# Optimization experiments

Measured on AMD Instinct MI355X. Metric: run time of the kernel, lower is better.

## Reference

```python
import jax, jax.numpy as jnp
import numpy as np
from jax import lax

G = 8        # group_num
BS = 32      # blocksize
SC = 13      # sample_channel = round(32*32*0.1/8)


def conv2d(x, w, b=None, stride=1, pad=0):
    y = lax.conv_general_dilated(x, w, (stride, stride), [(pad, pad), (pad, pad)],
                                 dimension_numbers=("NCHW", "OIHW", "NCHW"))
    if b is not None:
        y = y + b[None, :, None, None]
    return y


def prelu(x, a):
    return jnp.where(x >= 0, x, a * x)


def depth_to_space(x, bs):
    # matches Reshape_Concat_Adap: channel index = c_out*bs*bs + i*bs + j
    b, c, h, w = x.shape
    co = c // (bs * bs)
    x = x.reshape(b, co, bs, bs, h, w)
    x = x.transpose(0, 1, 4, 2, 5, 3)  # b, co, h, bs, w, bs
    return x.reshape(b, co, h * bs, w * bs)


def setup_inputs() -> dict:
    key = jax.random.key(0)
    ks = jax.random.split(key, 16)
    s = 0.05
    inp = {
        "x": jax.random.normal(ks[0], (8, 1, 256, 256), jnp.float32),
        "sample_w": jax.random.normal(ks[1], (G, SC, 1, BS, BS), jnp.float32) * 0.02,
        "up_w": jax.random.normal(ks[2], (G, BS * BS, SC, 1, 1), jnp.float32) * s,
        "up_b": jnp.zeros((G, BS * BS), jnp.float32),
        "conv1_w": jax.random.normal(ks[3], (G, 64, 1, 3, 3), jnp.float32) * s,
        "conv1_b": jnp.zeros((G, 64), jnp.float32),
        "conv1_a": jnp.full((G,), 0.25, jnp.float32),
        "fus_w": jax.random.normal(ks[4], (G - 1, 64, 128, 3, 3), jnp.float32) * s,
        "fus_b": jnp.zeros((G - 1, 64), jnp.float32),
        "fus_a": jnp.full((G - 1,), 0.25, jnp.float32),
        "t2_w": jax.random.normal(ks[5], (G, 64, 64, 3, 3), jnp.float32) * s,
        "t2_b": jnp.zeros((G, 64), jnp.float32),
        "t2_a": jnp.full((G,), 0.25, jnp.float32),
        "t3_w": jax.random.normal(ks[6], (G, 64, 64, 3, 3), jnp.float32) * s,
        "t3_b": jnp.zeros((G, 64), jnp.float32),
        "t3_a": jnp.full((G,), 0.25, jnp.float32),
        "t4_w": jax.random.normal(ks[7], (G, 64, 64, 3, 3), jnp.float32) * s,
        "t4_b": jnp.zeros((G, 64), jnp.float32),
        "t4_a": jnp.full((G,), 0.25, jnp.float32),
        "t5_w": jax.random.normal(ks[8], (G, 1, 64, 3, 3), jnp.float32) * s,
        "t5_b": jnp.zeros((G, 1), jnp.float32),
    }
    return inp


def reference(x, sample_w, up_w, up_b, conv1_w, conv1_b, conv1_a,
              fus_w, fus_b, fus_a, t2_w, t2_b, t2_a, t3_w, t3_b, t3_a,
              t4_w, t4_b, t4_a, t5_w, t5_b):
    def head(g):
        y = conv2d(x, sample_w[g], stride=BS)              # [B,SC,H/32,W/32]
        y = conv2d(y, up_w[g], up_b[g])                    # [B,1024,H/32,W/32]
        y = depth_to_space(y, BS)                          # [B,1,H,W]
        return prelu(conv2d(y, conv1_w[g], conv1_b[g], pad=1), conv1_a[g])

    def tail(h, g):
        h = prelu(conv2d(h, t2_w[g], t2_b[g], pad=1), t2_a[g])
        h = prelu(conv2d(h, t3_w[g], t3_b[g], pad=1), t3_a[g])
        h = prelu(conv2d(h, t4_w[g], t4_b[g], pad=1), t4_a[g])
        return conv2d(h, t5_w[g], t5_b[g], pad=1)          # [B,1,H,W]

    heads = [head(g) for g in range(G)]
    cur = heads[0]
    outs = [tail(cur, 0)]
    for m in range(G - 1):
        cat = jnp.concatenate([cur, heads[m + 1]], axis=1)  # [B,128,H,W]
        cur = prelu(conv2d(cat, fus_w[m], fus_b[m], pad=1), fus_a[m])
        outs.append(tail(cur, m + 1))
    return jnp.stack(outs, axis=0)  # [G,B,1,H,W]
```

## Files before the change

kernel.cpp:

```cpp
#include <hip/hip_runtime.h>
#include <stdint.h>

typedef __attribute__((ext_vector_type(8))) short short8;
typedef __attribute__((ext_vector_type(16))) float floatx16;

#define PLANE 16777216

__device__ __forceinline__ float b2f(short s) {
  union { uint32_t u; float f; } v; v.u = ((uint32_t)(uint16_t)s) << 16; return v.f;
}
__device__ __forceinline__ short f2b(float f) {
  union { float f; uint32_t u; } v; v.f = f;
  uint32_t r = (v.u + 0x7FFFu + ((v.u >> 16) & 1u)) >> 16;
  return (short)r;
}

__device__ __forceinline__ uint32_t ldsAddr(int r, int xp, int c) {
  uint32_t byte = ((uint32_t)(r * 258 + xp) << 6) + ((uint32_t)c << 1);
  byte ^= ((uint32_t)(xp & 7)) << 4;
  return byte;
}

template<int NCHUNK>
__global__ __launch_bounds__(512, 2)
void k_conv(const short* __restrict__ in1, const short* __restrict__ in2,
            const short* __restrict__ wp, const float* __restrict__ bias,
            const float* __restrict__ alpha, short* __restrict__ out)
{
  __shared__ __align__(16) uint8_t smem[4 * 258 * 64];
  const int wg = blockIdx.x;
  const int b = wg & 7;
  const int y0 = (wg >> 3) * 2;
  const int tid = threadIdx.x;
  const int l = tid & 63;
  const int w = tid >> 6;
  const int yrow = w & 1;
  const int pxq = w >> 1;
  const int lm = l & 31;
  const int lh = l >> 5;

  floatx16 acc[4];
  #pragma unroll
  for (int mf = 0; mf < 4; ++mf)
    #pragma unroll
    for (int r = 0; r < 16; ++r) acc[mf][r] = 0.f;

  const int xbase = pxq * 64 + lm;

  short8 stg[8];

  auto issue = [&](int q) {
    const short* __restrict__ src = ((q < 2) ? in1 : in2) + (size_t)(q & 1) * PLANE;
    #pragma unroll
    for (int i = 0; i < 8; ++i) {
      int widx = tid + i * 512;
      int r = widx >> 10;
      int xp = ((widx >> 2) & 255) + 1;
      int co = (widx & 3) << 3;
      int yy = y0 + r - 1;
      short8 v = {0, 0, 0, 0, 0, 0, 0, 0};
      if ((unsigned)yy < 256u)
        v = *(const short8*)(src + ((b * 256 + yy) * 256 + (xp - 1)) * 32 + co);
      stg[i] = v;
    }
  };
  auto commit = [&]() {
    #pragma unroll
    for (int i = 0; i < 8; ++i) {
      int widx = tid + i * 512;
      int r = widx >> 10;
      int xp = ((widx >> 2) & 255) + 1;
      int co = (widx & 3) << 3;
      *(short8*)(smem + ldsAddr(r, xp, co)) = stg[i];
    }
  };

  if (tid < 32) {
    short8 z = {0, 0, 0, 0, 0, 0, 0, 0};
    int r = tid >> 3;
    int xp = (tid & 4) ? 257 : 0;
    int co = (tid & 3) << 3;
    *(short8*)(smem + ldsAddr(r, xp, co)) = z;
  }

  issue(0);
  commit();
  __syncthreads();

  #pragma unroll
  for (int q = 0; q < NCHUNK; ++q) {
    if (q + 1 < NCHUNK) issue(q + 1);

    __builtin_amdgcn_s_setprio(1);
    #pragma unroll
    for (int ky = 0; ky < 3; ++ky)
    #pragma unroll
    for (int kx = 0; kx < 3; ++kx)
    #pragma unroll
    for (int s = 0; s < 2; ++s) {
      const int ks = (q * 9 + ky * 3 + kx) * 2 + s;
      const short8 bw0 = *(const short8*)(wp + ((ks * 2 + 0) * 64 + l) * 8);
      const short8 bw1 = *(const short8*)(wp + ((ks * 2 + 1) * 64 + l) * 8);
      const int cl = s * 16 + lh * 8;
      #pragma unroll
      for (int mf = 0; mf < 2; ++mf) {
        const int xp = xbase + mf * 32 + kx;
        const short8 av = *(const short8*)(smem + ldsAddr(yrow + ky, xp, cl));
        acc[mf * 2 + 0] = __builtin_amdgcn_mfma_f32_32x32x16_bf16(av, bw0, acc[mf * 2 + 0], 0, 0, 0);
        acc[mf * 2 + 1] = __builtin_amdgcn_mfma_f32_32x32x16_bf16(av, bw1, acc[mf * 2 + 1], 0, 0, 0);
      }
    }
    __builtin_amdgcn_s_setprio(0);

    if (q + 1 < NCHUNK) {
      __syncthreads();
      commit();
      __syncthreads();
    }
  }

  const float alp = alpha[0];
  const int y = y0 + yrow;
  #pragma unroll
  for (int nb = 0; nb < 2; ++nb) {
    const float bs = bias[nb * 32 + lm];
    short* __restrict__ op = out + (size_t)nb * PLANE + lm;
    #pragma unroll
    for (int mf = 0; mf < 2; ++mf) {
      #pragma unroll
      for (int r = 0; r < 16; ++r) {
        int px = pxq * 64 + mf * 32 + (r & 3) + ((r >> 2) << 3) + (lh << 2);
        float v = acc[mf * 2 + nb][r] + bs;
        v = v >= 0.f ? v : alp * v;
        op[((b * 256 + y) * 256 + px) * 32] = f2b(v);
      }
    }
  }
}

__global__ __launch_bounds__(256)
void k_pack(const float* __restrict__ w2, const float* __restrict__ w3,
            const float* __restrict__ w4, const float* __restrict__ wf,
            short* __restrict__ wp234, short* __restrict__ wpfus)
{
  int idx = blockIdx.x * 256 + threadIdx.x;
  if (idx < 24 * 36864) {
    int conv = idx / 36864;
    int r = idx - conv * 36864;
    int which = conv >> 3, g = conv & 7;
    const float* W = (which == 0 ? w2 : which == 1 ? w3 : w4) + g * 36864;
    int ks = r >> 10;
    int nblk = (r >> 9) & 1;
    int lane = (r >> 3) & 63;
    int e = r & 7;
    int q = ks / 18, tt = ks % 18;
    int t = tt >> 1, s = tt & 1;
    int cin = q * 32 + s * 16 + ((lane >> 5) << 3) + e;
    int cout = nblk * 32 + (lane & 31);
    int ky = t / 3, kx = t % 3;
    wp234[idx] = f2b(W[((cout * 64 + cin) * 3 + ky) * 3 + kx]);
  } else {
    int idx2 = idx - 24 * 36864;
    if (idx2 >= 7 * 73728) return;
    int conv = idx2 / 73728;
    int r = idx2 - conv * 73728;
    const float* W = wf + conv * 73728;
    int ks = r >> 10;
    int nblk = (r >> 9) & 1;
    int lane = (r >> 3) & 63;
    int e = r & 7;
    int q = ks / 18, tt = ks % 18;
    int t = tt >> 1, s = tt & 1;
    int cin = q * 32 + s * 16 + ((lane >> 5) << 3) + e;
    int cout = nblk * 32 + (lane & 31);
    int ky = t / 3, kx = t % 3;
    wpfus[idx2] = f2b(W[((cout * 128 + cin) * 3 + ky) * 3 + kx]);
  }
}

__global__ __launch_bounds__(256)
void k_sample(const float* __restrict__ x, const float* __restrict__ sw,
              float* __restrict__ s_all)
{
  int idx = blockIdx.x * 256 + threadIdx.x;
  int gx = idx & 7, gy = (idx >> 3) & 7;
  int t = idx >> 6;
  int c = t % 13; t /= 13;
  int b = t & 7, g = t >> 3;
  const float* xb = x + b * 65536 + (gy * 32) * 256 + gx * 32;
  const float* wp = sw + (g * 13 + c) * 1024;
  float acc = 0.f;
  for (int i = 0; i < 32; ++i) {
    #pragma unroll
    for (int j = 0; j < 32; ++j) acc += xb[i * 256 + j] * wp[i * 32 + j];
  }
  s_all[idx] = acc;
}

__global__ __launch_bounds__(256)
void k_upz(const float* __restrict__ s_all, const float* __restrict__ upw,
           const float* __restrict__ upb, float* __restrict__ z_all)
{
  int idx = blockIdx.x * 256 + threadIdx.x;
  int x = idx & 255, y = (idx >> 8) & 255;
  int b = (idx >> 16) & 7, g = idx >> 19;
  int pos = (y & 31) * 32 + (x & 31);
  int gy = y >> 5, gx = x >> 5;
  const float* sp = s_all + ((g * 8 + b) * 13) * 64 + gy * 8 + gx;
  const float* wp = upw + (g * 1024 + pos) * 13;
  float a = upb[g * 1024 + pos];
  #pragma unroll
  for (int c = 0; c < 13; ++c) a += wp[c] * sp[c * 64];
  z_all[idx] = a;
}

__global__ __launch_bounds__(256)
void k_conv1(const float* __restrict__ z, const float* __restrict__ w,
             const float* __restrict__ bias, const float* __restrict__ alpha,
             short* __restrict__ out)
{
  int wg = blockIdx.x;
  int b = wg & 7;
  int y = wg >> 3;
  int x = threadIdx.x;
  int pid = (b * 256 + y) * 256 + x;
  float zv[9];
  #pragma unroll
  for (int t = 0; t < 9; ++t) {
    int dy = t / 3, dx = t % 3;
    int yy = y + dy - 1, xx = x + dx - 1;
    zv[t] = ((unsigned)yy < 256u && (unsigned)xx < 256u)
              ? z[b * 65536 + yy * 256 + xx] : 0.f;
  }
  float alp = alpha[0];
  #pragma unroll
  for (int c0 = 0; c0 < 64; c0 += 8) {
    short8 pack;
    #pragma unroll
    for (int e = 0; e < 8; ++e) {
      int c = c0 + e;
      float a = bias[c];
      #pragma unroll
      for (int t = 0; t < 9; ++t) a += w[c * 9 + t] * zv[t];
      a = a >= 0.f ? a : alp * a;
      pack[e] = f2b(a);
    }
    *(short8*)(out + (size_t)(c0 >> 5) * PLANE + pid * 32 + (c0 & 31)) = pack;
  }
}

__global__ __launch_bounds__(256)
void k_t5(const short* __restrict__ in, const float* __restrict__ w,
          const float* __restrict__ bias, float* __restrict__ out)
{
  int wg = blockIdx.x;
  int b = wg & 7;
  int y = wg >> 3;
  int x = threadIdx.x;
  float acc = bias[0];
  for (int dy = 0; dy < 3; ++dy) {
    int yy = y + dy - 1;
    if ((unsigned)yy >= 256u) continue;
    for (int dx = 0; dx < 3; ++dx) {
      int xx = x + dx - 1;
      if ((unsigned)xx >= 256u) continue;
      const int pix = (b * 256 + yy) * 256 + xx;
      #pragma unroll
      for (int c0 = 0; c0 < 64; c0 += 8) {
        short8 v = *(const short8*)(in + (size_t)(c0 >> 5) * PLANE + pix * 32 + (c0 & 31));
        #pragma unroll
        for (int e = 0; e < 8; ++e)
          acc += w[(c0 + e) * 9 + dy * 3 + dx] * b2f(v[e]);
      }
    }
  }
  out[(b * 256 + y) * 256 + x] = acc;
}

extern "C" void kernel_launch(void* const* d_in, const int* in_sizes, int n_in,
                              void* d_out, int out_size, void* d_ws, size_t ws_size,
                              hipStream_t stream) {
  const float* X   = (const float*)d_in[0];
  const float* SW  = (const float*)d_in[1];
  const float* UPW = (const float*)d_in[2];
  const float* UPB = (const float*)d_in[3];
  const float* C1W = (const float*)d_in[4];
  const float* C1B = (const float*)d_in[5];
  const float* C1A = (const float*)d_in[6];
  const float* FW  = (const float*)d_in[7];
  const float* FB  = (const float*)d_in[8];
  const float* FA  = (const float*)d_in[9];
  const float* W2  = (const float*)d_in[10];
  const float* B2  = (const float*)d_in[11];
  const float* A2  = (const float*)d_in[12];
  const float* W3  = (const float*)d_in[13];
  const float* B3  = (const float*)d_in[14];
  const float* A3  = (const float*)d_in[15];
  const float* W4  = (const float*)d_in[16];
  const float* B4  = (const float*)d_in[17];
  const float* A4  = (const float*)d_in[18];
  const float* W5  = (const float*)d_in[19];
  const float* B5  = (const float*)d_in[20];
  float* OUT = (float*)d_out;
  (void)in_sizes; (void)n_in; (void)out_size; (void)ws_size;

  uint8_t* base = (uint8_t*)d_ws;
  size_t off = 0;
  auto alloc = [&](size_t bytes) -> uint8_t* {
    uint8_t* r = base + off;
    off += (bytes + 255) & ~(size_t)255;
    return r;
  };
  const size_t ACT_ELEMS = 2ull * PLANE;
  short* act[3];
  for (int i = 0; i < 3; ++i) act[i] = (short*)alloc(ACT_ELEMS * 2);
  float* z_all = (float*)alloc(4194304ull * 4);
  float* s_all = (float*)alloc(53248ull * 4);
  short* wp234 = (short*)alloc(884736ull * 2);
  short* wpfus = (short*)alloc(516096ull * 2);

  k_pack<<<dim3(5472), dim3(256), 0, stream>>>(W2, W3, W4, FW, wp234, wpfus);
  k_sample<<<dim3(208), dim3(256), 0, stream>>>(X, SW, s_all);
  k_upz<<<dim3(16384), dim3(256), 0, stream>>>(s_all, UPW, UPB, z_all);

  int cur = 0, A = 1, B = 2;
  k_conv1<<<dim3(2048), dim3(256), 0, stream>>>(z_all, C1W, C1B, C1A, act[cur]);

  for (int m = 0; m < 8; ++m) {
    const short* wp_t2 = wp234 + (0 * 8 + m) * 36864;
    const short* wp_t3 = wp234 + (1 * 8 + m) * 36864;
    const short* wp_t4 = wp234 + (2 * 8 + m) * 36864;

    k_conv<2><<<dim3(1024), dim3(512), 0, stream>>>(
        act[cur], act[cur], wp_t2, B2 + m * 64, A2 + m, act[A]);
    k_conv<2><<<dim3(1024), dim3(512), 0, stream>>>(
        act[A], act[A], wp_t3, B3 + m * 64, A3 + m, act[B]);
    k_conv<2><<<dim3(1024), dim3(512), 0, stream>>>(
        act[B], act[B], wp_t4, B4 + m * 64, A4 + m, act[A]);
    k_t5<<<dim3(2048), dim3(256), 0, stream>>>(
        act[A], W5 + m * 576, B5 + m, OUT + (size_t)m * 524288);

    if (m < 7) {
      k_conv1<<<dim3(2048), dim3(256), 0, stream>>>(
          z_all + (size_t)(m + 1) * 524288, C1W + (m + 1) * 576,
          C1B + (m + 1) * 64, C1A + (m + 1), act[B]);
      k_conv<4><<<dim3(1024), dim3(512), 0, stream>>>(
          act[cur], act[B], wpfus + m * 73728, FB + m * 64, FA + m, act[A]);
      int tmp = cur; cur = A; A = tmp;
    }
  }
}
```

Baseline: 3.098 ms.

## Shrink conv tile to one output row per workgroup, doubling grid

Each conv workgroup now computes one output row instead of two. That needs only three halo input rows in LDS instead of four, and each wave holds two accumulators instead of four. The grid doubles to 2048 workgroups. The aim is more parallelism and lower LDS and register use per workgroup, but each input row is now loaded about three times instead of twice, and weight reuse per LDS load goes down.

```diff
diff --git a/kernel.cpp b/kernel.cpp
--- a/kernel.cpp
+++ b/kernel.cpp
@@ -27,37 +27,35 @@
             const short* __restrict__ wp, const float* __restrict__ bias,
             const float* __restrict__ alpha, short* __restrict__ out)
 {
-  __shared__ __align__(16) uint8_t smem[4 * 258 * 64];
+  __shared__ __align__(16) uint8_t smem[3 * 258 * 64];
   const int wg = blockIdx.x;
   const int b = wg & 7;
-  const int y0 = (wg >> 3) * 2;
+  const int y = wg >> 3;
   const int tid = threadIdx.x;
   const int l = tid & 63;
   const int w = tid >> 6;
-  const int yrow = w & 1;
-  const int pxq = w >> 1;
   const int lm = l & 31;
   const int lh = l >> 5;
 
-  floatx16 acc[4];
-  #pragma unroll
-  for (int mf = 0; mf < 4; ++mf)
-    #pragma unroll
-    for (int r = 0; r < 16; ++r) acc[mf][r] = 0.f;
-
-  const int xbase = pxq * 64 + lm;
-
-  short8 stg[8];
+  floatx16 acc[2];
+  #pragma unroll
+  for (int nb = 0; nb < 2; ++nb)
+    #pragma unroll
+    for (int r = 0; r < 16; ++r) acc[nb][r] = 0.f;
+
+  const int xbase = w * 32 + lm;
+
+  short8 stg[6];
 
   auto issue = [&](int q) {
     const short* __restrict__ src = ((q < 2) ? in1 : in2) + (size_t)(q & 1) * PLANE;
     #pragma unroll
-    for (int i = 0; i < 8; ++i) {
+    for (int i = 0; i < 6; ++i) {
       int widx = tid + i * 512;
       int r = widx >> 10;
       int xp = ((widx >> 2) & 255) + 1;
       int co = (widx & 3) << 3;
-      int yy = y0 + r - 1;
+      int yy = y + r - 1;
       short8 v = {0, 0, 0, 0, 0, 0, 0, 0};
       if ((unsigned)yy < 256u)
         v = *(const short8*)(src + ((b * 256 + yy) * 256 + (xp - 1)) * 32 + co);
@@ -66,7 +64,7 @@
   };
   auto commit = [&]() {
     #pragma unroll
-    for (int i = 0; i < 8; ++i) {
+    for (int i = 0; i < 6; ++i) {
       int widx = tid + i * 512;
       int r = widx >> 10;
       int xp = ((widx >> 2) & 255) + 1;
@@ -75,7 +73,7 @@
     }
   };
 
-  if (tid < 32) {
+  if (tid < 24) {
     short8 z = {0, 0, 0, 0, 0, 0, 0, 0};
     int r = tid >> 3;
     int xp = (tid & 4) ? 257 : 0;
@@ -102,13 +100,10 @@
       const short8 bw0 = *(const short8*)(wp + ((ks * 2 + 0) * 64 + l) * 8);
       const short8 bw1 = *(const short8*)(wp + ((ks * 2 + 1) * 64 + l) * 8);
       const int cl = s * 16 + lh * 8;
-      #pragma unroll
-      for (int mf = 0; mf < 2; ++mf) {
-        const int xp = xbase + mf * 32 + kx;
-        const short8 av = *(const short8*)(smem + ldsAddr(yrow + ky, xp, cl));
-        acc[mf * 2 + 0] = __builtin_amdgcn_mfma_f32_32x32x16_bf16(av, bw0, acc[mf * 2 + 0], 0, 0, 0);
-        acc[mf * 2 + 1] = __builtin_amdgcn_mfma_f32_32x32x16_bf16(av, bw1, acc[mf * 2 + 1], 0, 0, 0);
-      }
+      const int xp = xbase + kx;
+      const short8 av = *(const short8*)(smem + ldsAddr(ky, xp, cl));
+      acc[0] = __builtin_amdgcn_mfma_f32_32x32x16_bf16(av, bw0, acc[0], 0, 0, 0);
+      acc[1] = __builtin_amdgcn_mfma_f32_32x32x16_bf16(av, bw1, acc[1], 0, 0, 0);
     }
     __builtin_amdgcn_s_setprio(0);
 
@@ -120,20 +115,16 @@
   }
 
   const float alp = alpha[0];
-  const int y = y0 + yrow;
   #pragma unroll
   for (int nb = 0; nb < 2; ++nb) {
     const float bs = bias[nb * 32 + lm];
     short* __restrict__ op = out + (size_t)nb * PLANE + lm;
     #pragma unroll
-    for (int mf = 0; mf < 2; ++mf) {
-      #pragma unroll
-      for (int r = 0; r < 16; ++r) {
-        int px = pxq * 64 + mf * 32 + (r & 3) + ((r >> 2) << 3) + (lh << 2);
-        float v = acc[mf * 2 + nb][r] + bs;
-        v = v >= 0.f ? v : alp * v;
-        op[((b * 256 + y) * 256 + px) * 32] = f2b(v);
-      }
+    for (int r = 0; r < 16; ++r) {
+      int px = w * 32 + (r & 3) + ((r >> 2) << 3) + (lh << 2);
+      float v = acc[nb][r] + bs;
+      v = v >= 0.f ? v : alp * v;
+      op[((b * 256 + y) * 256 + px) * 32] = f2b(v);
     }
   }
 }
@@ -331,11 +322,11 @@
     const short* wp_t3 = wp234 + (1 * 8 + m) * 36864;
     const short* wp_t4 = wp234 + (2 * 8 + m) * 36864;
 
-    k_conv<2><<<dim3(1024), dim3(512), 0, stream>>>(
+    k_conv<2><<<dim3(2048), dim3(512), 0, stream>>>(
         act[cur], act[cur], wp_t2, B2 + m * 64, A2 + m, act[A]);
-    k_conv<2><<<dim3(1024), dim3(512), 0, stream>>>(
+    k_conv<2><<<dim3(2048), dim3(512), 0, stream>>>(
         act[A], act[A], wp_t3, B3 + m * 64, A3 + m, act[B]);
-    k_conv<2><<<dim3(1024), dim3(512), 0, stream>>>(
+    k_conv<2><<<dim3(2048), dim3(512), 0, stream>>>(
         act[B], act[B], wp_t4, B4 + m * 64, A4 + m, act[A]);
     k_t5<<<dim3(2048), dim3(256), 0, stream>>>(
         act[A], W5 + m * 576, B5 + m, OUT + (size_t)m * 524288);
@@ -344,7 +335,7 @@
       k_conv1<<<dim3(2048), dim3(256), 0, stream>>>(
           z_all + (size_t)(m + 1) * 524288, C1W + (m + 1) * 576,
           C1B + (m + 1) * 64, C1A + (m + 1), act[B]);
-      k_conv<4><<<dim3(1024), dim3(512), 0, stream>>>(
+      k_conv<4><<<dim3(2048), dim3(512), 0, stream>>>(
           act[cur], act[B], wpfus + m * 73728, FB + m * 64, FA + m, act[A]);
       int tmp = cur; cur = A; A = tmp;
     }
```

New measurement: 2.908 ms. -6.1%, faster.
